# Performance work log

Measured on AMD Instinct MI355X. Metric: run time of the kernel, lower is better.

## Reference

```python
import jax, jax.numpy as jnp
import numpy as np

N_FEATURES = 256
RAND_RANGE = 100.0


def _random_embed(x):
    """Deterministic pseudo-random embedding: each scalar in x seeds a counter-based
    RNG producing N_FEATURES uniforms in [0, RAND_RANGE). (JAX threefry replaces
    Python's Mersenne Twister; same structure: value-seeded deterministic uniforms.)"""
    flat = jax.lax.stop_gradient(x).reshape(-1)
    seeds = jax.lax.bitcast_convert_type(flat, jnp.uint32)  # value -> integer seed
    base = jax.random.key(42)
    keys = jax.vmap(lambda s: jax.random.fold_in(base, s))(seeds)
    emb = jax.vmap(lambda k: jax.random.uniform(k, (N_FEATURES,), minval=0.0, maxval=RAND_RANGE))(keys)
    return emb.reshape(x.shape + (N_FEATURES,))  # [B, S, F]


def setup_inputs() -> dict:
    key = jax.random.key(0)
    kx, kw, kb = jax.random.split(key, 3)
    x = jax.random.normal(kx, (256, 512), dtype=jnp.float32)
    W = jax.random.normal(kw, (N_FEATURES, N_FEATURES), dtype=jnp.float32) * 0.05
    b = jax.random.normal(kb, (N_FEATURES,), dtype=jnp.float32) * 0.05
    return {"x": x, "W": W, "b": b}


def reference(x, W, b):
    emb = _random_embed(x)                      # [B, S, F]
    out = jnp.einsum('bsf,gf->bsg', emb, W) + b  # nn.Linear: emb @ W.T + b
    return out
```

## Files before the change

kernel.cpp:

```cpp
#include <hip/hip_runtime.h>
#include <stdint.h>

#define F 256
#define R 64
#define THREADS 256
#define GCH 32
#define NCH (F / GCH)
#define CH_SLOTS (GCH * F / 8)
#define NBUF 3

typedef __attribute__((ext_vector_type(8))) short short8;
typedef __attribute__((ext_vector_type(4))) float floatx4;

__device__ __forceinline__ uint32_t rotl32(uint32_t x, int d) {
  return __builtin_amdgcn_alignbit(x, x, (uint32_t)(32 - d));
}

struct TFK { uint32_t k0, k1, k2, a1, a2, a3, a4, a5; };

__device__ __forceinline__ TFK mkkeys(uint32_t k0, uint32_t k1) {
  TFK K;
  K.k0 = k0; K.k1 = k1; K.k2 = k0 ^ k1 ^ 0x1BD11BDAu;
  K.a1 = K.k2 + 1u; K.a2 = k0 + 2u; K.a3 = k1 + 3u;
  K.a4 = K.k2 + 4u; K.a5 = k0 + 5u;
  return K;
}

__device__ __forceinline__ void tf_one(const TFK& K, uint32_t& x0, uint32_t& x1) {
  x0 += K.k0; x1 += K.k1;
#define TF1(r) x0 += x1; x1 = rotl32(x1, r); x1 ^= x0;
  TF1(13) TF1(15) TF1(26) TF1(6)   x0 += K.k1; x1 += K.a1;
  TF1(17) TF1(29) TF1(16) TF1(24)  x0 += K.k2; x1 += K.a2;
  TF1(13) TF1(15) TF1(26) TF1(6)   x0 += K.k0; x1 += K.a3;
  TF1(17) TF1(29) TF1(16) TF1(24)  x0 += K.k1; x1 += K.a4;
  TF1(13) TF1(15) TF1(26) TF1(6)   x0 += K.k2; x1 += K.a5;
#undef TF1
}

__device__ __forceinline__ void tf_pair(const TFK& K, uint32_t i,
                                        uint32_t& oa, uint32_t& ob) {
  uint32_t a0 = K.k0, a1 = K.k1 + i;
  uint32_t b0 = K.k0, b1 = K.k1 + i + 1u;
#define TF2(r)  a0 += a1; b0 += b1;                         \
                a1 = rotl32(a1, r); b1 = rotl32(b1, r);     \
                a1 ^= a0; b1 ^= b0;
#define INJ2(u, v) a0 += (u); b0 += (u); a1 += (v); b1 += (v);
  TF2(13) TF2(15) TF2(26) TF2(6)   INJ2(K.k1, K.a1)
  TF2(17) TF2(29) TF2(16) TF2(24)  INJ2(K.k2, K.a2)
  TF2(13) TF2(15) TF2(26) TF2(6)   INJ2(K.k0, K.a3)
  TF2(17) TF2(29) TF2(16) TF2(24)  INJ2(K.k1, K.a4)
  TF2(13) TF2(15) TF2(26) TF2(6)   INJ2(K.k2, K.a5)
#undef TF2
#undef INJ2
  oa = a0 ^ a1;
  ob = b0 ^ b1;
}

__device__ __forceinline__ uint32_t featpack(const TFK& K, uint32_t i) {
  uint32_t xa, xb;
  tf_pair(K, i, xa, xb);
  uint32_t ulo = __float_as_uint((float)xa * 2.3283064365386963e-8f);
  uint32_t uhi = __float_as_uint((float)xb * 2.3283064365386963e-8f);
  ulo += 0x7FFFu + ((ulo >> 16) & 1u);
  uhi += 0x7FFFu + ((uhi >> 16) & 1u);
  return __builtin_amdgcn_perm(uhi, ulo, 0x07060302u);
}

__device__ __forceinline__ short8 quad(const TFK& K, uint32_t fb) {
  uint32_t w32[4];
  #pragma unroll
  for (int p = 0; p < 4; ++p) w32[p] = featpack(K, fb + 2u * p);
  union { uint32_t w[4]; short8 s; } u;
  u.w[0] = w32[0]; u.w[1] = w32[1]; u.w[2] = w32[2]; u.w[3] = w32[3];
  return u.s;
}

__device__ __forceinline__ uint32_t f2bf(float f) {
  uint32_t u = __float_as_uint(f);
  u += 0x7FFFu + ((u >> 16) & 1u);
  return u >> 16;
}

__device__ __forceinline__ void gl_lds16(const void* gptr, void* lptr) {
  __builtin_amdgcn_global_load_lds(
      (const __attribute__((address_space(1))) uint32_t*)gptr,
      (__attribute__((address_space(3))) uint32_t*)lptr, 16, 0, 0);
}

__device__ __forceinline__ void dma_chunk(const uint16_t* __restrict__ src,
                                          uint16_t* dst, int wave, int lane) {
  #pragma unroll
  for (int it = 0; it < CH_SLOTS / THREADS; ++it) {
    int sbase = it * THREADS + wave * 64;
    gl_lds16(src + (size_t)(sbase + lane) * 8, dst + (size_t)sbase * 8);
  }
}

__global__ __launch_bounds__(256) void femb_conv(const float* __restrict__ W,
                                                 uint16_t* __restrict__ ws) {
  int s = blockIdx.x * 256 + threadIdx.x;
  int gt = s >> 10;
  int c = (s >> 5) & 31;
  int g = s & 31;
  const float4* src = (const float4*)(W + (size_t)(gt * GCH + g) * F + c * 8);
  float4 v0 = src[0], v1 = src[1];
  short8 o;
  o[0] = (short)f2bf(v0.x); o[1] = (short)f2bf(v0.y);
  o[2] = (short)f2bf(v0.z); o[3] = (short)f2bf(v0.w);
  o[4] = (short)f2bf(v1.x); o[5] = (short)f2bf(v1.y);
  o[6] = (short)f2bf(v1.z); o[7] = (short)f2bf(v1.w);
  *(short8*)(ws + (size_t)s * 8) = o;
}

__global__ __launch_bounds__(THREADS, 3) void femb_main(
    const float* __restrict__ x, const uint16_t* __restrict__ Wbf,
    const float* __restrict__ bias, float* __restrict__ out) {
  __shared__ uint16_t sW[NBUF][GCH * F];

  const int tid  = threadIdx.x;
  const int lane = tid & 63;
  const int wave = tid >> 6;
  const int qd   = lane >> 4;
  const int l16  = lane & 15;
  const size_t row0 = (size_t)blockIdx.x * R;
  const int myrow = (int)row0 + wave * 16 + l16;

  float xv = x[myrow];

  dma_chunk(Wbf, sW[0], wave, lane);
  dma_chunk(Wbf + (size_t)CH_SLOTS * 8, sW[1], wave, lane);

  float bgv[16];
  #pragma unroll
  for (int n = 0; n < 16; ++n) bgv[n] = bias[n * 16 + l16];

  const TFK K42 = mkkeys(0u, 42u);
  uint32_t u0 = 0u, u1 = __float_as_uint(xv);
  tf_one(K42, u0, u1);
  const TFK K = mkkeys(u0, u1);

  short8 afrag[8];
  #pragma unroll
  for (int kt = 0; kt < 8; ++kt)
    afrag[kt] = quad(K, (uint32_t)(kt * 32 + qd * 8));

  floatx4 acc[16];
  #pragma unroll
  for (int n = 0; n < 16; ++n) acc[n] = (floatx4){0.f, 0.f, 0.f, 0.f};

  #pragma unroll
  for (int gt = 0; gt < NCH; ++gt) {
    __builtin_amdgcn_sched_barrier(0);
    if (gt == NCH - 1)
      asm volatile("s_waitcnt vmcnt(0) lgkmcnt(0)" ::: "memory");
    else
      asm volatile("s_waitcnt vmcnt(4) lgkmcnt(0)" ::: "memory");
    __builtin_amdgcn_s_barrier();
    __builtin_amdgcn_sched_barrier(0);

    if (gt + 2 < NCH)
      dma_chunk(Wbf + (size_t)(gt + 2) * CH_SLOTS * 8,
                sW[(gt + 2) % NBUF], wave, lane);

    const uint16_t* buf = sW[gt % NBUF];
    #pragma unroll
    for (int kt = 0; kt < 8; ++kt) {
      int c = kt * 4 + qd;
      #pragma unroll
      for (int n = 0; n < 2; ++n) {
        short8 b = *(const short8*)&buf[(size_t)(c * 32 + n * 16 + l16) * 8];
        acc[gt * 2 + n] = __builtin_amdgcn_mfma_f32_16x16x32_bf16(
            afrag[kt], b, acc[gt * 2 + n], 0, 0, 0);
      }
    }
  }

  const size_t growbase = row0 + (size_t)(wave * 16 + qd * 4);
  #pragma unroll
  for (int n = 0; n < 16; ++n) {
    int g = n * 16 + l16;
    #pragma unroll
    for (int reg = 0; reg < 4; ++reg)
      out[(growbase + reg) * F + g] = acc[n][reg] + bgv[n];
  }
}

extern "C" void kernel_launch(void* const* d_in, const int* in_sizes, int n_in,
                              void* d_out, int out_size, void* d_ws, size_t ws_size,
                              hipStream_t stream) {
  const float* x = (const float*)d_in[0];
  const float* W = (const float*)d_in[1];
  const float* b = (const float*)d_in[2];
  float* out = (float*)d_out;
  uint16_t* wsbf = (uint16_t*)d_ws;
  const int nrows = in_sizes[0];
  const int blocks = nrows / R;

  hipLaunchKernelGGL(femb_conv, dim3((F * F / 8) / 256), dim3(256), 0, stream, W, wsbf);
  hipLaunchKernelGGL(femb_main, dim3(blocks), dim3(THREADS), 0, stream,
                     x, wsbf, b, out);
}
```

Before: 189.7 us.

## Stream W by K-chunks and interleave threefry generation with MFMA

Reorders the main loop to iterate over K slices instead of output-column chunks. Each step DMAs a K-slice of W covering all 256 outputs and runs 16 MFMAs against one A fragment. The threefry/bf16 packing for the next K-slice is interleaved between the MFMA groups, so RNG ALU work overlaps matrix work. Only one A fragment stays live instead of eight, which lowers register pressure. The outer loop is no longer unrolled, which adds loop overhead and a per-step dependency on the freshly generated fragment.

```diff
diff --git a/kernel.cpp b/kernel.cpp
--- a/kernel.cpp
+++ b/kernel.cpp
@@ -4,9 +4,8 @@
 #define F 256
 #define R 64
 #define THREADS 256
-#define GCH 32
-#define NCH (F / GCH)
-#define CH_SLOTS (GCH * F / 8)
+#define NCH 8
+#define CH_SLOTS 1024
 #define NBUF 3
 
 typedef __attribute__((ext_vector_type(8))) short short8;
@@ -87,22 +86,13 @@
       (__attribute__((address_space(3))) uint32_t*)lptr, 16, 0, 0);
 }
 
-__device__ __forceinline__ void dma_chunk(const uint16_t* __restrict__ src,
-                                          uint16_t* dst, int wave, int lane) {
-  #pragma unroll
-  for (int it = 0; it < CH_SLOTS / THREADS; ++it) {
-    int sbase = it * THREADS + wave * 64;
-    gl_lds16(src + (size_t)(sbase + lane) * 8, dst + (size_t)sbase * 8);
-  }
-}
-
 __global__ __launch_bounds__(256) void femb_conv(const float* __restrict__ W,
                                                  uint16_t* __restrict__ ws) {
   int s = blockIdx.x * 256 + threadIdx.x;
   int gt = s >> 10;
   int c = (s >> 5) & 31;
   int g = s & 31;
-  const float4* src = (const float4*)(W + (size_t)(gt * GCH + g) * F + c * 8);
+  const float4* src = (const float4*)(W + (size_t)(gt * 32 + g) * F + c * 8);
   float4 v0 = src[0], v1 = src[1];
   short8 o;
   o[0] = (short)f2bf(v0.x); o[1] = (short)f2bf(v0.y);
@@ -112,10 +102,22 @@
   *(short8*)(ws + (size_t)s * 8) = o;
 }
 
+__device__ __forceinline__ void dma_kchunk(const uint16_t* __restrict__ Wbf,
+                                           int kt, uint16_t* dst,
+                                           int wave, int lane) {
+  #pragma unroll
+  for (int it = 0; it < CH_SLOTS / THREADS; ++it) {
+    int Lb = it * THREADS + wave * 64;
+    const uint16_t* g = Wbf +
+        (size_t)((Lb >> 7) * 8192 + kt * 1024 + (Lb & 127) * 8);
+    gl_lds16(g + (size_t)lane * 8, dst + (size_t)Lb * 8);
+  }
+}
+
 __global__ __launch_bounds__(THREADS, 3) void femb_main(
     const float* __restrict__ x, const uint16_t* __restrict__ Wbf,
     const float* __restrict__ bias, float* __restrict__ out) {
-  __shared__ uint16_t sW[NBUF][GCH * F];
+  __shared__ uint16_t sW[NBUF][CH_SLOTS * 8];
 
   const int tid  = threadIdx.x;
   const int lane = tid & 63;
@@ -126,52 +128,58 @@
   const int myrow = (int)row0 + wave * 16 + l16;
 
   float xv = x[myrow];
-
-  dma_chunk(Wbf, sW[0], wave, lane);
-  dma_chunk(Wbf + (size_t)CH_SLOTS * 8, sW[1], wave, lane);
-
   float bgv[16];
   #pragma unroll
   for (int n = 0; n < 16; ++n) bgv[n] = bias[n * 16 + l16];
+
+  dma_kchunk(Wbf, 0, sW[0], wave, lane);
+  dma_kchunk(Wbf, 1, sW[1], wave, lane);
 
   const TFK K42 = mkkeys(0u, 42u);
   uint32_t u0 = 0u, u1 = __float_as_uint(xv);
   tf_one(K42, u0, u1);
   const TFK K = mkkeys(u0, u1);
 
-  short8 afrag[8];
-  #pragma unroll
-  for (int kt = 0; kt < 8; ++kt)
-    afrag[kt] = quad(K, (uint32_t)(kt * 32 + qd * 8));
+  short8 afragC = quad(K, (uint32_t)(qd * 8));
 
   floatx4 acc[16];
   #pragma unroll
   for (int n = 0; n < 16; ++n) acc[n] = (floatx4){0.f, 0.f, 0.f, 0.f};
 
-  #pragma unroll
-  for (int gt = 0; gt < NCH; ++gt) {
+  #pragma unroll 1
+  for (int kt = 0; kt < NCH; ++kt) {
     __builtin_amdgcn_sched_barrier(0);
-    if (gt == NCH - 1)
+    if (kt == NCH - 1)
       asm volatile("s_waitcnt vmcnt(0) lgkmcnt(0)" ::: "memory");
     else
       asm volatile("s_waitcnt vmcnt(4) lgkmcnt(0)" ::: "memory");
     __builtin_amdgcn_s_barrier();
     __builtin_amdgcn_sched_barrier(0);
 
-    if (gt + 2 < NCH)
-      dma_chunk(Wbf + (size_t)(gt + 2) * CH_SLOTS * 8,
-                sW[(gt + 2) % NBUF], wave, lane);
-
-    const uint16_t* buf = sW[gt % NBUF];
+    if (kt + 2 < NCH)
+      dma_kchunk(Wbf, kt + 2, sW[(kt + 2) % NBUF], wave, lane);
+
+    const uint16_t* bp = &sW[kt % NBUF][(size_t)(qd * 256 + l16 * 8)];
+    const uint32_t fb = (uint32_t)((kt + 1) * 32 + qd * 8);
+    const bool more = (kt + 1 < NCH);
+    uint32_t w32[4];
+
     #pragma unroll
-    for (int kt = 0; kt < 8; ++kt) {
-      int c = kt * 4 + qd;
+    for (int q = 0; q < 4; ++q) {
       #pragma unroll
-      for (int n = 0; n < 2; ++n) {
-        short8 b = *(const short8*)&buf[(size_t)(c * 32 + n * 16 + l16) * 8];
-        acc[gt * 2 + n] = __builtin_amdgcn_mfma_f32_16x16x32_bf16(
-            afrag[kt], b, acc[gt * 2 + n], 0, 0, 0);
+      for (int h = 0; h < 4; ++h) {
+        int n2 = q * 4 + h;
+        short8 b = *(const short8*)(bp + (n2 >> 1) * 1024 + (n2 & 1) * 128);
+        acc[n2] = __builtin_amdgcn_mfma_f32_16x16x32_bf16(afragC, b, acc[n2],
+                                                          0, 0, 0);
       }
+      if (more) w32[q] = featpack(K, fb + 2u * q);
+    }
+
+    if (more) {
+      union { uint32_t w[4]; short8 s; } u;
+      u.w[0] = w32[0]; u.w[1] = w32[1]; u.w[2] = w32[2]; u.w[3] = w32[3];
+      afragC = u.s;
     }
   }
 
```

Measured after the change: 215.5 us. 1.14x slower.
